# Performance work log

Measured on AMD Instinct MI355X. Metric: run time of the kernel, lower is better.

Reference implementation:

```python
import jax, jax.numpy as jnp
import numpy as np

N_NODES = 100000
N_EDGES = 1600000
IN_DIM = 64
EDGE_DIM = 8
H1, H2 = 128, 64
FEAT = 2 * IN_DIM + EDGE_DIM  # 136


def setup_inputs() -> dict:
    key = jax.random.key(0)
    ks = jax.random.split(key, 9)
    z = jax.random.normal(ks[0], (N_NODES, IN_DIM), dtype=jnp.float32)
    edge_index = jax.random.randint(ks[1], (2, N_EDGES), 0, N_NODES, dtype=jnp.int64)
    edge_attr = jax.random.normal(ks[2], (N_EDGES, EDGE_DIM), dtype=jnp.float32)
    # MLP params (Linear stores weight as [out, in]; we keep [in, out] for x @ W)
    def lin(k, fan_in, fan_out):
        bound = 1.0 / np.sqrt(fan_in)
        kw, kb = jax.random.split(k)
        W = jax.random.uniform(kw, (fan_in, fan_out), minval=-bound, maxval=bound, dtype=jnp.float32)
        b = jax.random.uniform(kb, (fan_out,), minval=-bound, maxval=bound, dtype=jnp.float32)
        return W, b
    W1, b1 = lin(ks[3], FEAT, H1)
    W2, b2 = lin(ks[4], H1, H2)
    W3, b3 = lin(ks[5], H2, 1)
    return {"z": z, "edge_index": edge_index, "edge_attr": edge_attr,
            "W1": W1, "b1": b1, "W2": W2, "b2": b2, "W3": W3, "b3": b3}


def reference(z, edge_index, edge_attr, W1, b1, W2, b2, W3, b3):
    src, dst = edge_index[0], edge_index[1]
    # gather node embeddings per edge and concat with edge attributes: [E, 2*D+A]
    feat = jnp.concatenate([z[src], z[dst], edge_attr], axis=-1)
    h = jax.nn.relu(feat @ W1 + b1)   # Dropout is identity in eval mode
    h = jax.nn.relu(h @ W2 + b2)
    logits = (h @ W3 + b3).squeeze(-1)  # [E]
    return logits
```

## Files before the change

kernel.cpp:

```cpp
#include <hip/hip_runtime.h>
#include <hip/hip_bf16.h>
#include <stdint.h>
#include <stddef.h>

#define NODES 100000
#define EDGES 1600000
#define NPB 64
#define EDGE_GRID 1250
#define NCHUNK 6250

typedef float f4 __attribute__((ext_vector_type(4)));
typedef float f32x4 __attribute__((ext_vector_type(4)));
typedef short s8v __attribute__((ext_vector_type(8)));
typedef unsigned short u16x8 __attribute__((ext_vector_type(8)));

__device__ __forceinline__ float bf2f(unsigned short u) {
  union { unsigned int i; float f; } v; v.i = ((unsigned int)u) << 16; return v.f;
}
__device__ __forceinline__ unsigned short f2bf(float f) {
  union { float f; unsigned int i; } v; v.f = f;
  return (unsigned short)((v.i + 0x7FFFu + ((v.i >> 16) & 1u)) >> 16);
}
__device__ __forceinline__ short f2bf_hw(float x) {
  __hip_bfloat16 h = __float2bfloat16(x);
  union { __hip_bfloat16 h; short s; } u; u.h = h; return u.s;
}

__device__ __forceinline__ int pqperm(int jj) {
  return (jj & 0x60) | ((jj & 0x0C) << 1) | ((jj & 0x10) >> 2) | (jj & 3);
}

__global__ __launch_bounds__(256) void node_pq_kernel(
    const float* __restrict__ z, const float* __restrict__ W1,
    const float* __restrict__ b1, unsigned short* __restrict__ PQ) {
  __shared__ float sz[NPB * 64];
  const int t = threadIdx.x;
  const int n0 = blockIdx.x * NPB;
#pragma unroll
  for (int it = 0; it < 4; ++it) {
    int idx = it * 256 + t;
    int node = n0 + (idx >> 4);
    f4 v = {0.f, 0.f, 0.f, 0.f};
    if (node < NODES) v = ((const f4*)z)[(size_t)node * 16 + (idx & 15)];
    ((f4*)sz)[idx] = v;
  }
  const int j = t;
  const int jj = (j < 128) ? j : (j - 128);
  const int outcol = (j < 128) ? pqperm(jj) : (128 + pqperm(jj));
  const float* wbase = (j < 128) ? (W1 + jj) : (W1 + 64 * 128 + jj);
  float wcol[64];
#pragma unroll
  for (int k = 0; k < 64; ++k) wcol[k] = wbase[(size_t)k * 128];
  const float bias = (j < 128) ? b1[jj] : 0.f;
  __syncthreads();
#pragma unroll 1
  for (int n = 0; n < NPB; ++n) {
    if (n0 + n >= NODES) break;
    const f4* zr = (const f4*)(sz + n * 64);
    float a = bias;
#pragma unroll
    for (int k4 = 0; k4 < 16; ++k4) {
      f4 zv = zr[k4];
      a = fmaf(zv[0], wcol[k4 * 4 + 0], a);
      a = fmaf(zv[1], wcol[k4 * 4 + 1], a);
      a = fmaf(zv[2], wcol[k4 * 4 + 2], a);
      a = fmaf(zv[3], wcol[k4 * 4 + 3], a);
    }
    PQ[(size_t)(n0 + n) * 256 + outcol] = f2bf(a);
  }
}

__global__ __launch_bounds__(256) void edge_mfma_kernel(
    const int* __restrict__ eidx, const float* __restrict__ eattr,
    const float* __restrict__ W1, const float* __restrict__ W2,
    const float* __restrict__ b2, const float* __restrict__ W3,
    const float* __restrict__ b3,
    const unsigned short* __restrict__ PQ, float* __restrict__ out) {
  const int t = threadIdx.x;
  const int lane = t & 63;
  const int w = t >> 6;
  const int r = lane & 15;
  const int g = lane >> 4;

  s8v bfrag[4][4];
#pragma unroll
  for (int kt = 0; kt < 4; ++kt)
#pragma unroll
    for (int nt = 0; nt < 4; ++nt) {
      s8v f;
#pragma unroll
      for (int jx = 0; jx < 8; ++jx) {
        int h = jx >> 2, jp = jx & 3;
        int jjv = 32 * kt + 16 * h + 4 * g + jp;
        f[jx] = (short)f2bf(W2[(size_t)jjv * 64 + nt * 16 + r]);
      }
      bfrag[kt][nt] = f;
    }
  s8v w1cf[8];
#pragma unroll
  for (int mt = 0; mt < 8; ++mt) {
    s8v f = {0, 0, 0, 0, 0, 0, 0, 0};
    if (g == 0) {
#pragma unroll
      for (int jx = 0; jx < 8; ++jx)
        f[jx] = (short)f2bf(W1[(size_t)(128 + jx) * 128 + 16 * mt + r]);
    }
    w1cf[mt] = f;
  }
  float b2v[4], w3v[4];
#pragma unroll
  for (int nt = 0; nt < 4; ++nt) { b2v[nt] = b2[nt * 16 + r]; w3v[nt] = W3[nt * 16 + r]; }
  const float bias3 = b3[0];
  const f32x4 zc = {0.f, 0.f, 0.f, 0.f};

#pragma unroll 1
  for (int chunk = blockIdx.x; chunk < NCHUNK; chunk += EDGE_GRID) {
    const int ebase = chunk * 256 + w * 64;
    const int src_all = eidx[ebase + lane];
    const int dst_all = eidx[EDGES + ebase + lane];
    unsigned int ea_pk[4];
    {
      const f4* eap = (const f4*)(eattr + (size_t)(ebase + lane) * 8);
      f4 a0 = eap[0], a1 = eap[1];
      ea_pk[0] = (unsigned int)(unsigned short)f2bf_hw(a0[0]) |
                 ((unsigned int)(unsigned short)f2bf_hw(a0[1]) << 16);
      ea_pk[1] = (unsigned int)(unsigned short)f2bf_hw(a0[2]) |
                 ((unsigned int)(unsigned short)f2bf_hw(a0[3]) << 16);
      ea_pk[2] = (unsigned int)(unsigned short)f2bf_hw(a1[0]) |
                 ((unsigned int)(unsigned short)f2bf_hw(a1[1]) << 16);
      ea_pk[3] = (unsigned int)(unsigned short)f2bf_hw(a1[2]) |
                 ((unsigned int)(unsigned short)f2bf_hw(a1[3]) << 16);
    }

#pragma unroll
    for (int st = 0; st < 4; ++st) {
      const int e0 = ebase + st * 16;
      const int idx = st * 16 + r;
      const int srcv = __shfl(src_all, idx, 64);
      const int dstv = __shfl(dst_all, idx, 64);
      s8v eaf;
#pragma unroll
      for (int c = 0; c < 4; ++c) {
        unsigned int pk = (unsigned int)__shfl((int)ea_pk[c], idx, 64);
        eaf[2 * c] = (short)(pk & 0xFFFFu);
        eaf[2 * c + 1] = (short)(pk >> 16);
      }
      const unsigned short* Pb = PQ + (size_t)srcv * 256 + 8 * g;
      const unsigned short* Qb = PQ + (size_t)dstv * 256 + 128 + 8 * g;
      u16x8 p[4], q[4];
#pragma unroll
      for (int kt = 0; kt < 4; ++kt) {
        p[kt] = *(const u16x8*)(Pb + 32 * kt);
        q[kt] = *(const u16x8*)(Qb + 32 * kt);
      }
      f32x4 acc[4] = {zc, zc, zc, zc};
#pragma unroll
      for (int kt = 0; kt < 4; ++kt) {
        f32x4 E0 = __builtin_amdgcn_mfma_f32_16x16x32_bf16(w1cf[2 * kt], eaf, zc, 0, 0, 0);
        f32x4 E1 = __builtin_amdgcn_mfma_f32_16x16x32_bf16(w1cf[2 * kt + 1], eaf, zc, 0, 0, 0);
        s8v af;
#pragma unroll
        for (int jp = 0; jp < 4; ++jp) {
          float s0 = bf2f(p[kt][jp]) + bf2f(q[kt][jp]) + E0[jp];
          af[jp] = f2bf_hw(fmaxf(s0, 0.f));
          float s1 = bf2f(p[kt][4 + jp]) + bf2f(q[kt][4 + jp]) + E1[jp];
          af[4 + jp] = f2bf_hw(fmaxf(s1, 0.f));
        }
#pragma unroll
        for (int nt = 0; nt < 4; ++nt)
          acc[nt] = __builtin_amdgcn_mfma_f32_16x16x32_bf16(af, bfrag[kt][nt], acc[nt], 0, 0, 0);
      }
      float pr0 = 0.f, pr1 = 0.f, pr2 = 0.f, pr3 = 0.f;
#pragma unroll
      for (int nt = 0; nt < 4; ++nt) {
        pr0 = fmaf(fmaxf(acc[nt][0] + b2v[nt], 0.f), w3v[nt], pr0);
        pr1 = fmaf(fmaxf(acc[nt][1] + b2v[nt], 0.f), w3v[nt], pr1);
        pr2 = fmaf(fmaxf(acc[nt][2] + b2v[nt], 0.f), w3v[nt], pr2);
        pr3 = fmaf(fmaxf(acc[nt][3] + b2v[nt], 0.f), w3v[nt], pr3);
      }
#pragma unroll
      for (int m = 1; m < 16; m <<= 1) {
        pr0 += __shfl_xor(pr0, m, 64);
        pr1 += __shfl_xor(pr1, m, 64);
        pr2 += __shfl_xor(pr2, m, 64);
        pr3 += __shfl_xor(pr3, m, 64);
      }
      if (r < 4) {
        float v = (r == 0) ? pr0 : (r == 1) ? pr1 : (r == 2) ? pr2 : pr3;
        out[e0 + 4 * g + r] = v + bias3;
      }
    }
  }
}

extern "C" void kernel_launch(void* const* d_in, const int* in_sizes, int n_in,
                              void* d_out, int out_size, void* d_ws, size_t ws_size,
                              hipStream_t stream) {
  const float* z     = (const float*)d_in[0];
  const int*   eidx  = (const int*)d_in[1];
  const float* eattr = (const float*)d_in[2];
  const float* W1    = (const float*)d_in[3];
  const float* b1    = (const float*)d_in[4];
  const float* W2    = (const float*)d_in[5];
  const float* b2    = (const float*)d_in[6];
  const float* W3    = (const float*)d_in[7];
  const float* b3    = (const float*)d_in[8];
  float* out = (float*)d_out;

  unsigned short* PQ = (unsigned short*)d_ws;
  node_pq_kernel<<<(NODES + NPB - 1) / NPB, 256, 0, stream>>>(z, W1, b1, PQ);
  edge_mfma_kernel<<<EDGE_GRID, 256, 0, stream>>>(
      eidx, eattr, W1, W2, b2, W3, b3, PQ, out);
}
```

Baseline: 213.6 us.

## Use MFMA for node projection and identity-MFMA for P+Q gather sum

Replaces the scalar FMA node projection kernel with a per-wave 16-node MFMA tile that uses split bf16 (hi/lo) products to approximate fp32 accuracy, and drops the column permutation of PQ. In the edge kernel, the P+Q+E sum is computed with an identity-matrix MFMA over the gathered bf16 vectors instead of per-element VALU bf16-to-float adds, and each lane group now loads either P or Q rows. Edge grid size is raised. This trades VALU work for extra matrix instructions and changes the PQ layout, so the ordering must stay consistent across the two kernels.

```diff
diff --git a/kernel.cpp b/kernel.cpp
--- a/kernel.cpp
+++ b/kernel.cpp
@@ -5,9 +5,9 @@
 
 #define NODES 100000
 #define EDGES 1600000
-#define NPB 64
-#define EDGE_GRID 1250
 #define NCHUNK 6250
+#define EDGE_GRID 3125
+#define NTILES 6250
 
 typedef float f4 __attribute__((ext_vector_type(4)));
 typedef float f32x4 __attribute__((ext_vector_type(4)));
@@ -26,47 +26,56 @@
   union { __hip_bfloat16 h; short s; } u; u.h = h; return u.s;
 }
 
-__device__ __forceinline__ int pqperm(int jj) {
-  return (jj & 0x60) | ((jj & 0x0C) << 1) | ((jj & 0x10) >> 2) | (jj & 3);
-}
-
-__global__ __launch_bounds__(256) void node_pq_kernel(
+__global__ __launch_bounds__(256) void node_pq_mfma(
     const float* __restrict__ z, const float* __restrict__ W1,
     const float* __restrict__ b1, unsigned short* __restrict__ PQ) {
-  __shared__ float sz[NPB * 64];
   const int t = threadIdx.x;
-  const int n0 = blockIdx.x * NPB;
-#pragma unroll
-  for (int it = 0; it < 4; ++it) {
-    int idx = it * 256 + t;
-    int node = n0 + (idx >> 4);
-    f4 v = {0.f, 0.f, 0.f, 0.f};
-    if (node < NODES) v = ((const f4*)z)[(size_t)node * 16 + (idx & 15)];
-    ((f4*)sz)[idx] = v;
-  }
-  const int j = t;
-  const int jj = (j < 128) ? j : (j - 128);
-  const int outcol = (j < 128) ? pqperm(jj) : (128 + pqperm(jj));
-  const float* wbase = (j < 128) ? (W1 + jj) : (W1 + 64 * 128 + jj);
-  float wcol[64];
-#pragma unroll
-  for (int k = 0; k < 64; ++k) wcol[k] = wbase[(size_t)k * 128];
-  const float bias = (j < 128) ? b1[jj] : 0.f;
-  __syncthreads();
+  const int lane = t & 63;
+  const int w = t >> 6;
+  const int r = lane & 15, g = lane >> 4;
+  const int tile = blockIdx.x * 4 + w;
+  if (tile >= NTILES) return;
+  const int n0 = tile * 16;
+
+  s8v a_hi[2], a_lo[2];
+#pragma unroll
+  for (int kt = 0; kt < 2; ++kt) {
+    const f4* zp = (const f4*)(z + (size_t)(n0 + r) * 64 + 32 * kt + 8 * g);
+    f4 z0 = zp[0], z1 = zp[1];
+    float zv[8] = {z0[0], z0[1], z0[2], z0[3], z1[0], z1[1], z1[2], z1[3]};
+    s8v hi, lo;
+#pragma unroll
+    for (int jx = 0; jx < 8; ++jx) {
+      short h = f2bf_hw(zv[jx]);
+      hi[jx] = h;
+      lo[jx] = f2bf_hw(zv[jx] - bf2f((unsigned short)h));
+    }
+    a_hi[kt] = hi; a_lo[kt] = lo;
+  }
+
 #pragma unroll 1
-  for (int n = 0; n < NPB; ++n) {
-    if (n0 + n >= NODES) break;
-    const f4* zr = (const f4*)(sz + n * 64);
-    float a = bias;
-#pragma unroll
-    for (int k4 = 0; k4 < 16; ++k4) {
-      f4 zv = zr[k4];
-      a = fmaf(zv[0], wcol[k4 * 4 + 0], a);
-      a = fmaf(zv[1], wcol[k4 * 4 + 1], a);
-      a = fmaf(zv[2], wcol[k4 * 4 + 2], a);
-      a = fmaf(zv[3], wcol[k4 * 4 + 3], a);
-    }
-    PQ[(size_t)(n0 + n) * 256 + outcol] = f2bf(a);
+  for (int nt = 0; nt < 16; ++nt) {
+    const int col = (nt & 7) * 16 + r;
+    const int rowbase = (nt < 8) ? 0 : 64;
+    const float init = (nt < 8) ? b1[col] : 0.f;
+    f32x4 acc = {init, init, init, init};
+#pragma unroll
+    for (int kt = 0; kt < 2; ++kt) {
+      s8v whi, wlo;
+#pragma unroll
+      for (int jx = 0; jx < 8; ++jx) {
+        float wv = W1[(size_t)(rowbase + 32 * kt + 8 * g + jx) * 128 + col];
+        short h = f2bf_hw(wv);
+        whi[jx] = h;
+        wlo[jx] = f2bf_hw(wv - bf2f((unsigned short)h));
+      }
+      acc = __builtin_amdgcn_mfma_f32_16x16x32_bf16(a_hi[kt], whi, acc, 0, 0, 0);
+      acc = __builtin_amdgcn_mfma_f32_16x16x32_bf16(a_lo[kt], whi, acc, 0, 0, 0);
+      acc = __builtin_amdgcn_mfma_f32_16x16x32_bf16(a_hi[kt], wlo, acc, 0, 0, 0);
+    }
+#pragma unroll
+    for (int reg = 0; reg < 4; ++reg)
+      PQ[(size_t)(n0 + 4 * g + reg) * 256 + nt * 16 + r] = f2bf(acc[reg]);
   }
 }
 
@@ -107,6 +116,9 @@
     }
     w1cf[mt] = f;
   }
+  s8v a_id = {0, 0, 0, 0, 0, 0, 0, 0};
+  if ((g & 1) == (r >> 3)) a_id[r & 7] = (short)0x3F80;
+
   float b2v[4], w3v[4];
 #pragma unroll
   for (int nt = 0; nt < 4; ++nt) { b2v[nt] = b2[nt * 16 + r]; w3v[nt] = W3[nt * 16 + r]; }
@@ -138,33 +150,33 @@
       const int idx = st * 16 + r;
       const int srcv = __shfl(src_all, idx, 64);
       const int dstv = __shfl(dst_all, idx, 64);
-      s8v eaf;
-#pragma unroll
-      for (int c = 0; c < 4; ++c) {
-        unsigned int pk = (unsigned int)__shfl((int)ea_pk[c], idx, 64);
-        eaf[2 * c] = (short)(pk & 0xFFFFu);
-        eaf[2 * c + 1] = (short)(pk >> 16);
-      }
-      const unsigned short* Pb = PQ + (size_t)srcv * 256 + 8 * g;
-      const unsigned short* Qb = PQ + (size_t)dstv * 256 + 128 + 8 * g;
-      u16x8 p[4], q[4];
+      union { unsigned int u[4]; s8v v; } eau;
+#pragma unroll
+      for (int c = 0; c < 4; ++c) eau.u[c] = (unsigned int)__shfl((int)ea_pk[c], idx, 64);
+      const s8v eaf = eau.v;
+
+      const unsigned short* base =
+          (g < 2) ? (PQ + (size_t)srcv * 256 + 8 * (g & 1))
+                  : (PQ + (size_t)dstv * 256 + 128 + 8 * (g & 1));
+      u16x8 bpq[8];
 #pragma unroll
       for (int kt = 0; kt < 4; ++kt) {
-        p[kt] = *(const u16x8*)(Pb + 32 * kt);
-        q[kt] = *(const u16x8*)(Qb + 32 * kt);
-      }
+        bpq[2 * kt]     = *(const u16x8*)(base + 32 * kt);
+        bpq[2 * kt + 1] = *(const u16x8*)(base + 32 * kt + 16);
+      }
+
       f32x4 acc[4] = {zc, zc, zc, zc};
 #pragma unroll
       for (int kt = 0; kt < 4; ++kt) {
         f32x4 E0 = __builtin_amdgcn_mfma_f32_16x16x32_bf16(w1cf[2 * kt], eaf, zc, 0, 0, 0);
         f32x4 E1 = __builtin_amdgcn_mfma_f32_16x16x32_bf16(w1cf[2 * kt + 1], eaf, zc, 0, 0, 0);
+        f32x4 S0 = __builtin_amdgcn_mfma_f32_16x16x32_bf16(a_id, (s8v)bpq[2 * kt], E0, 0, 0, 0);
+        f32x4 S1 = __builtin_amdgcn_mfma_f32_16x16x32_bf16(a_id, (s8v)bpq[2 * kt + 1], E1, 0, 0, 0);
         s8v af;
 #pragma unroll
         for (int jp = 0; jp < 4; ++jp) {
-          float s0 = bf2f(p[kt][jp]) + bf2f(q[kt][jp]) + E0[jp];
-          af[jp] = f2bf_hw(fmaxf(s0, 0.f));
-          float s1 = bf2f(p[kt][4 + jp]) + bf2f(q[kt][4 + jp]) + E1[jp];
-          af[4 + jp] = f2bf_hw(fmaxf(s1, 0.f));
+          af[jp]     = f2bf_hw(fmaxf(S0[jp], 0.f));
+          af[4 + jp] = f2bf_hw(fmaxf(S1[jp], 0.f));
         }
 #pragma unroll
         for (int nt = 0; nt < 4; ++nt)
@@ -208,7 +220,7 @@
   float* out = (float*)d_out;
 
   unsigned short* PQ = (unsigned short*)d_ws;
-  node_pq_kernel<<<(NODES + NPB - 1) / NPB, 256, 0, stream>>>(z, W1, b1, PQ);
+  node_pq_mfma<<<(NTILES + 3) / 4, 256, 0, stream>>>(z, W1, b1, PQ);
   edge_mfma_kernel<<<EDGE_GRID, 256, 0, stream>>>(
       eidx, eattr, W1, W2, b2, W3, b3, PQ, out);
 }
```

After: 201.3 us. 1.06x faster.
